# Kernel tuning notes

Hardware: AMD Instinct MI355X
Metric: run time of the kernel (lower is better)

Reference implementation:

```python
import jax, jax.numpy as jnp
import numpy as np

B, K, N, D, H, NNEG, NTOP = 8, 8, 128, 256, 128, 64, 64
UNARY_SCALES = (1.0, 1.0, 1.0)  # one scale per tree level, tree_height = log2(K) = 3


def setup_inputs():
    key = jax.random.key(0)
    ks = jax.random.split(key, 8)
    s = 0.05
    return {
        'pos_fea': jax.random.normal(ks[0], (B, K, N, D), jnp.float32),
        'neg_fea': jax.random.normal(ks[1], (B * K, NNEG, D), jnp.float32),
        'pos_classes': jax.random.randint(ks[2], (B, K, N), 0, 20),
        'target_class': jax.random.randint(ks[3], (B,), 0, 20),
        'Wp1': jax.random.normal(ks[4], (2 * D, H), jnp.float32) * s,
        'bp1': jnp.zeros((H,), jnp.float32),
        'Wp2': jax.random.normal(ks[5], (H, 1), jnp.float32) * s,
        'bp2': jnp.zeros((1,), jnp.float32),
        'Wu1': jax.random.normal(ks[6], (2 * D, H), jnp.float32) * s,
        'bu1': jnp.zeros((H,), jnp.float32),
        'Wu2': jax.random.normal(ks[7], (H, 1), jnp.float32) * s,
        'bu2': jnp.zeros((1,), jnp.float32),
    }


def _relation(f0, f1, W1, b1, W2, b2):
    # RelationModule: Dense(H, relu) -> Dense(1) applied to concat([f0_m, f1_n])
    # for every cross pair; concat-Dense is split into two GEMMs. -> [Bn, M0, M1]
    d = f0.shape[-1]
    h0 = jnp.einsum('bmd,dh->bmh', f0, W1[:d])
    h1 = jnp.einsum('bnd,dh->bnh', f1, W1[d:])
    h = jax.nn.relu(h0[:, :, None, :] + h1[:, None, :, :] + b1)
    return jnp.einsum('bmnh,h->bmn', h, W2[:, 0]) + b2[0]


def _bg(t, idx):
    # batched_gather along axis 1: t [Bn, P, ...], idx [Bn, T]
    ie = idx.reshape(idx.shape + (1,) * (t.ndim - 2))
    ie = jnp.broadcast_to(ie, idx.shape + t.shape[2:])
    return jnp.take_along_axis(t, ie, axis=1)


def _rep(fea, sub):
    # subproblem representative feature: fea [Bn,S,N,D], sub [Bn,M,S] -> [Bn,M,D]
    idx = jnp.swapaxes(sub, 1, 2)[..., None]              # [Bn,S,M,1]
    idx = jnp.broadcast_to(idx, idx.shape[:-1] + (fea.shape[-1],))
    return jnp.take_along_axis(fea, idx, axis=2).mean(axis=1)


def _tree(pos_fea, neg_fea, Wp1, bp1, Wp2, bp2, Wu1, bu1, Wu2, bu2):
    pos_flat = pos_fea.reshape(B * K, N, D)
    # UnaryModule: mean relation score of each positive proposal vs the negative bag
    ue = _relation(pos_flat, neg_fea, Wu1, bu1, Wu2, bu2).mean(-1)   # [B*K, N]
    sub = jnp.broadcast_to(jnp.arange(N, dtype=jnp.int32)[None, :, None], (B * K, N, 1))
    pe = jnp.zeros_like(ue)
    tree_height = int(np.log2(K))
    best = None
    for i in range(tree_height):
        S = 2 ** i                      # subproblem size per branch at this level
        Bn = sub.shape[0] // 2
        M = sub.shape[1]
        sub2 = sub.reshape(Bn, 2, M, S)  # [::2] / [1::2] split of adjacent rows
        sub0, sub1 = sub2[:, 0], sub2[:, 1]
        pe2 = pe.reshape(Bn, 2, M)
        ue2 = ue.reshape(Bn, 2, M)
        fea = pos_flat.reshape(Bn, 2, S, N, D)
        rep0 = _rep(fea[:, 0], sub0)
        rep1 = _rep(fea[:, 1], sub1)
        # PairwiseCrossSimilarity: scores for all cross pairs of candidates
        scores = _relation(rep0, rep1, Wp1, bp1, Wp2, bp2).reshape(Bn, M * M)
        p0 = jnp.repeat(jnp.arange(M), M)
        p1 = jnp.tile(jnp.arange(M), M)
        pe = pe2[:, 0][:, p0] + pe2[:, 1][:, p1] - scores
        ue = ue2[:, 0][:, p0] + ue2[:, 1][:, p1]
        total = pe + UNARY_SCALES[i] * ue
        sub = jnp.concatenate([sub0[:, p0], sub1[:, p1]], axis=-1)  # [Bn, M*M, 2S]
        topk = 1 if i == tree_height - 1 else min(M * M, NTOP)
        _, inds = jax.lax.top_k(-total, topk)
        sub = _bg(sub, inds)
        ue = jnp.take_along_axis(ue, inds, axis=1)
        pe = jnp.take_along_axis(pe, inds, axis=1)
        best = jnp.take_along_axis(total, inds, axis=1)
    return sub, best


def reference(pos_fea, neg_fea, pos_classes, target_class,
              Wp1, bp1, Wp2, bp2, Wu1, bu1, Wu2, bu2):
    sub, _ = _tree(pos_fea, neg_fea, Wp1, bp1, Wp2, bp2, Wu1, bu1, Wu2, bu2)
    is_target = (pos_classes == target_class[:, None, None]).astype(jnp.float32)
    return sub[:, 0], is_target  # selected proposal per image [B,K], [B,K,N]
```

## Files before the change

kernel.cpp:

```cpp
#include <hip/hip_runtime.h>
#include <stdint.h>

#define B_ 8
#define K_ 8
#define N_ 128
#define D_ 256
#define H_ 128
#define NNEG_ 64

typedef unsigned long long u64;
typedef float f4 __attribute__((ext_vector_type(4)));

typedef const __attribute__((address_space(1))) void gvoid;
typedef __attribute__((address_space(3))) void lvoid;
#define G2L(gsrc, ldst) \
    __builtin_amdgcn_global_load_lds((gvoid*)(gsrc), (lvoid*)(ldst), 16, 0, 0)

__device__ __forceinline__ u64 shfl_xor_u64(u64 v, int m) {
    int lo = __shfl_xor((int)(unsigned)v, m, 64);
    int hi = __shfl_xor((int)(unsigned)(v >> 32), m, 64);
    return ((u64)(unsigned)hi << 32) | (unsigned)lo;
}
__device__ __forceinline__ u64 bitonic_merge64(u64 m, int lane) {
#pragma unroll
    for (int j = 32; j > 0; j >>= 1) {
        u64 o = shfl_xor_u64(m, j);
        bool keepMin = ((lane & j) == 0);
        bool lt = m < o;
        m = (keepMin == lt) ? m : o;
    }
    return m;
}
__device__ __forceinline__ u64 merge2(u64 a, u64 b, int lane) {
    u64 br = shfl_xor_u64(b, 63);
    u64 m = a < br ? a : br;
    return bitonic_merge64(m, lane);
}
__device__ __forceinline__ unsigned sortable(float f) {
    unsigned u = __float_as_uint(f);
    return (u & 0x80000000u) ? ~u : (u | 0x80000000u);
}
__device__ __forceinline__ float unsortable(unsigned u) {
    return __uint_as_float((u & 0x80000000u) ? (u & 0x7FFFFFFFu) : ~u);
}
__device__ __forceinline__ void sort128_reg(u64& v0, u64& v1, int lane) {
#pragma unroll
    for (int k = 2; k <= 64; k <<= 1) {
        bool d0 = ((lane & k) == 0);
        bool d1 = (k == 64) ? false : d0;
#pragma unroll
        for (int j = k >> 1; j > 0; j >>= 1) {
            u64 o0 = shfl_xor_u64(v0, j);
            bool km0 = (((lane & j) == 0) == d0);
            v0 = (km0 == (v0 < o0)) ? v0 : o0;
            u64 o1 = shfl_xor_u64(v1, j);
            bool km1 = (((lane & j) == 0) == d1);
            v1 = (km1 == (v1 < o1)) ? v1 : o1;
        }
    }
    if (v0 > v1) { u64 tmp = v0; v0 = v1; v1 = tmp; }
#pragma unroll
    for (int j = 32; j > 0; j >>= 1) {
        bool km = ((lane & j) == 0);
        u64 o0 = shfl_xor_u64(v0, j);
        v0 = (km == (v0 < o0)) ? v0 : o0;
        u64 o1 = shfl_xor_u64(v1, j);
        v1 = (km == (v1 < o1)) ? v1 : o1;
    }
}

__global__ __launch_bounds__(64) void g1_gemm(
    const float* __restrict__ pos, const float* __restrict__ neg,
    const float* __restrict__ Wu1, const float* __restrict__ Wp1,
    const int* __restrict__ pos_classes, const int* __restrict__ target_class,
    float* __restrict__ HU0, float* __restrict__ HU1n,
    float* __restrict__ HP0, float* __restrict__ HP1,
    float* __restrict__ outp) {
    int bid = blockIdx.x;
    int t = threadIdx.x;
    if (bid >= 896) {
        int base = (bid - 896) * 2048 + t * 32;
#pragma unroll
        for (int q = 0; q < 32; ++q) {
            int idx = base + q;
            outp[64 + idx] = (pos_classes[idx] == target_class[idx >> 10]) ? 1.0f : 0.0f;
        }
        return;
    }
    const float* A; const float* W; float* OUT; int bid2;
    if (bid < 256)      { A = pos; W = Wu1;           OUT = HU0;  bid2 = bid; }
    else if (bid < 384) { A = neg; W = Wu1 + D_ * H_; OUT = HU1n; bid2 = bid - 256; }
    else if (bid < 640) { A = pos; W = Wp1;           OUT = HP0;  bid2 = bid - 384; }
    else                { A = pos; W = Wp1 + D_ * H_; OUT = HP1;  bid2 = bid - 640; }
    int rb = (bid2 >> 1) * 64;
    int cb64 = (bid2 & 1) * 64;

    __shared__ __align__(16) float AsL[2][64 * 32];
    __shared__ __align__(16) float BsL[2][32 * 64];
    int tx = t & 7, ty = t >> 3;
    f4 acc[8][2];
#pragma unroll
    for (int i = 0; i < 8; ++i) { acc[i][0] = (f4)0.f; acc[i][1] = (f4)0.f; }

#pragma unroll
    for (int rep = 0; rep < 8; ++rep) {
        int flat = rep * 64 + t;
        int row = flat >> 3;
        int kq = (flat & 7) ^ ((flat >> 5) & 7);
        G2L(&A[(size_t)(rb + row) * D_ + kq * 4], &AsL[0][rep * 256]);
    }
#pragma unroll
    for (int rep = 0; rep < 8; ++rep) {
        int flat = rep * 64 + t;
        int kr = flat >> 4, cq = flat & 15;
        G2L(&W[(size_t)kr * H_ + cb64 + cq * 4], &BsL[0][rep * 256]);
    }
    __syncthreads();

    for (int chunk = 0; chunk < 8; ++chunk) {
        int cur = chunk & 1, nxt = cur ^ 1;
        if (chunk < 7) {
            int k0n = (chunk + 1) * 32;
#pragma unroll
            for (int rep = 0; rep < 8; ++rep) {
                int flat = rep * 64 + t;
                int row = flat >> 3;
                int kq = (flat & 7) ^ ((flat >> 5) & 7);
                G2L(&A[(size_t)(rb + row) * D_ + k0n + kq * 4], &AsL[nxt][rep * 256]);
            }
#pragma unroll
            for (int rep = 0; rep < 8; ++rep) {
                int flat = rep * 64 + t;
                int kr = flat >> 4, cq = flat & 15;
                G2L(&W[(size_t)(k0n + kr) * H_ + cb64 + cq * 4], &BsL[nxt][rep * 256]);
            }
        }
#pragma unroll
        for (int g = 0; g < 8; ++g) {
            f4 av[8];
#pragma unroll
            for (int i = 0; i < 8; ++i) {
                int row = ty * 8 + i;
                int qp = g ^ ((2 * ty + (i >> 2)) & 7);
                av[i] = *(const f4*)&AsL[cur][row * 32 + qp * 4];
            }
#pragma unroll
            for (int q = 0; q < 4; ++q) {
                f4 b0 = *(const f4*)&BsL[cur][(g * 4 + q) * 64 + tx * 8];
                f4 b1 = *(const f4*)&BsL[cur][(g * 4 + q) * 64 + tx * 8 + 4];
#pragma unroll
                for (int i = 0; i < 8; ++i) {
                    float a = av[i][q];
                    acc[i][0][0] += a * b0[0]; acc[i][0][1] += a * b0[1];
                    acc[i][0][2] += a * b0[2]; acc[i][0][3] += a * b0[3];
                    acc[i][1][0] += a * b1[0]; acc[i][1][1] += a * b1[1];
                    acc[i][1][2] += a * b1[2]; acc[i][1][3] += a * b1[3];
                }
            }
        }
        __syncthreads();
    }
#pragma unroll
    for (int i = 0; i < 8; ++i) {
        *(f4*)&OUT[(size_t)(rb + ty * 8 + i) * H_ + cb64 + tx * 8] = acc[i][0];
        *(f4*)&OUT[(size_t)(rb + ty * 8 + i) * H_ + cb64 + tx * 8 + 4] = acc[i][1];
    }
}

__global__ __launch_bounds__(128) void g2_ue_sc0(
    const float* __restrict__ HU0, const float* __restrict__ HU1n,
    const float* __restrict__ bu1, const float* __restrict__ Wu2,
    const float* __restrict__ bu2v,
    const float* __restrict__ HP0, const float* __restrict__ HP1,
    const float* __restrict__ bp1, const float* __restrict__ Wp2,
    const float* __restrict__ bp2,
    float* __restrict__ t0, float* __restrict__ sc0) {
    __shared__ float LsT[128][36];
    __shared__ float RsT[128][68];
    __shared__ float wsv[128];
    __shared__ float red[32][33];

    int bid = blockIdx.x;
    int t = threadIdx.x;
    bool is_ue = bid < 256;

    const float* Lsrc; const float* Rsrc; const float* b1v; const float* W2;
    if (is_ue) {
        int bk = bid >> 2, mt = bid & 3;
        Lsrc = HU0 + (size_t)(bk * N_ + mt * 32) * H_;
        Rsrc = HU1n + (size_t)bk * NNEG_ * H_;
        b1v = bu1; W2 = Wu2;
    } else {
        int bid2 = bid - 256;
        int b = bid2 >> 3, m0t = (bid2 >> 1) & 3, m1t = bid2 & 1;
        Lsrc = HP0 + (size_t)b * 2 * N_ * H_ + m0t * 32 * H_;
        Rsrc = HP1 + (size_t)b * 2 * N_ * H_ + N_ * H_ + m1t * 64 * H_;
        b1v = bp1; W2 = Wp2;
    }
    for (int i = t; i < 32 * 32; i += 128) {
        int m = i & 31, hq = i >> 5;
        const f4 a = *(const f4*)&Lsrc[(size_t)m * H_ + hq * 4];
        const f4 b = *(const f4*)&b1v[hq * 4];
        LsT[hq * 4 + 0][m] = a[0] + b[0];
        LsT[hq * 4 + 1][m] = a[1] + b[1];
        LsT[hq * 4 + 2][m] = a[2] + b[2];
        LsT[hq * 4 + 3][m] = a[3] + b[3];
    }
    for (int i = t; i < 64 * 32; i += 128) {
        int n = i & 63, hq = i >> 6;
        const f4 a = *(const f4*)&Rsrc[(size_t)n * H_ + hq * 4];
        RsT[hq * 4 + 0][n] = a[0];
        RsT[hq * 4 + 1][n] = a[1];
        RsT[hq * 4 + 2][n] = a[2];
        RsT[hq * 4 + 3][n] = a[3];
    }
    wsv[t] = W2[t];
    __syncthreads();

    int tm = t & 7, tn = t >> 3;
    f4 acc[4];
#pragma unroll
    for (int i = 0; i < 4; ++i) acc[i] = (f4)0.f;
#pragma unroll 2
    for (int hg = 0; hg < 32; ++hg) {
        f4 wv = *(const f4*)&wsv[hg * 4];
        f4 lv[4], rv[4];
#pragma unroll
        for (int s = 0; s < 4; ++s) {
            lv[s] = *(const f4*)&LsT[hg * 4 + s][tm * 4];
            rv[s] = *(const f4*)&RsT[hg * 4 + s][tn * 4];
        }
#pragma unroll
        for (int s = 0; s < 4; ++s) {
            float w = wv[s];
#pragma unroll
            for (int i = 0; i < 4; ++i) {
                float l = lv[s][i];
                float v;
                v = l + rv[s][0]; v = v > 0.f ? v : 0.f; acc[i][0] += v * w;
                v = l + rv[s][1]; v = v > 0.f ? v : 0.f; acc[i][1] += v * w;
                v = l + rv[s][2]; v = v > 0.f ? v : 0.f; acc[i][2] += v * w;
                v = l + rv[s][3]; v = v > 0.f ? v : 0.f; acc[i][3] += v * w;
            }
        }
    }

    if (is_ue) {
        int bk = bid >> 2, mt = bid & 3;
#pragma unroll
        for (int i = 0; i < 4; ++i) {
            red[tm * 4 + i][tn * 2 + 0] = acc[i][0] + acc[i][1];
            red[tm * 4 + i][tn * 2 + 1] = acc[i][2] + acc[i][3];
        }
        __syncthreads();
        if (t < 32) {
            float s = 0.f;
            for (int q = 0; q < 32; ++q) s += red[t][q];
            t0[bk * N_ + mt * 32 + t] = s * (1.0f / NNEG_) + bu2v[0];
        }
    } else {
        int bid2 = bid - 256;
        int b = bid2 >> 3, m0t = (bid2 >> 1) & 3, m1t = bid2 & 1;
        float bp2v = bp2[0];
        float* orow = sc0 + (size_t)b * 16384;
#pragma unroll
        for (int i = 0; i < 4; ++i) {
            int m0 = m0t * 32 + tm * 4 + i;
            int m1 = m1t * 64 + tn * 4;
            f4 o = {acc[i][0] + bp2v, acc[i][1] + bp2v,
                    acc[i][2] + bp2v, acc[i][3] + bp2v};
            *(f4*)&orow[m0 * 128 + m1] = o;
        }
    }
}

__global__ __launch_bounds__(256) void g3a_top0(const float* __restrict__ sc0,
                                                const float* __restrict__ t0,
                                                u64* __restrict__ g3c) {
    int bid = blockIdx.x;
    int r = bid >> 3, c = bid & 7;
    int t = threadIdx.x, lane = t & 63, w = t >> 6;
    __shared__ float tt[256];
    __shared__ u64 cand[4][128];
    if (t < 256) tt[t] = t0[r * 256 + t];
    __syncthreads();
    const float* row = sc0 + (size_t)r * 16384 + c * 2048 + w * 512;
    unsigned sv[8];
#pragma unroll
    for (int j = 0; j < 8; ++j) {
        int li = j * 64 + lane;
        int idx = c * 2048 + w * 512 + li;
        float v = (tt[idx >> 7] + tt[128 + (idx & 127)]) - row[li];
        sv[j] = sortable(v);
    }
    unsigned T = 0u;
#pragma unroll
    for (int it = 0; it < 16; ++it) {
        int p = 30 - 2 * it;
        unsigned C1 = T | (1u << p), C2 = T | (2u << p), C3 = T | (3u << p);
        unsigned c1 = 0u, c2 = 0u, c3 = 0u;
#pragma unroll
        for (int j = 0; j < 8; ++j) {
            c1 += (unsigned)__popcll(__ballot(sv[j] < C1));
            c2 += (unsigned)__popcll(__ballot(sv[j] < C2));
            c3 += (unsigned)__popcll(__ballot(sv[j] < C3));
        }
        unsigned k = (c3 < 64u) ? 3u : (c2 < 64u) ? 2u : (c1 < 64u) ? 1u : 0u;
        T |= (k << p);
    }
    u64* my = cand[w];
    int base = 0;
#pragma unroll
    for (int j = 0; j < 8; ++j) {
        u64 mask = __ballot(sv[j] <= T);
        if (sv[j] <= T) {
            int pos = base + (int)__popcll(mask & ((1ull << lane) - 1ull));
            if (pos < 128) {
                int idx = c * 2048 + w * 512 + j * 64 + lane;
                my[pos] = ((u64)sv[j] << 32) | (unsigned)idx;
            }
        }
        base += (int)__popcll(mask);
    }
    int cc = base < 128 ? base : 128;
    u64 v0 = (lane < cc) ? my[lane] : ~0ull;
    u64 v1 = (64 + lane < cc) ? my[64 + lane] : ~0ull;
    sort128_reg(v0, v1, lane);
    my[lane] = v0;
    __syncthreads();
    if (w == 0) {
        u64 x0 = cand[0][lane], x1 = cand[1][lane];
        u64 x2 = cand[2][lane], x3 = cand[3][lane];
        u64 y0 = merge2(x0, x1, lane), y1 = merge2(x2, x3, lane);
        g3c[(size_t)bid * 64 + lane] = merge2(y0, y1, lane);
    }
}

__global__ __launch_bounds__(256) void g4a_s1(
    const float* __restrict__ HP0, const float* __restrict__ HP1,
    const u64* __restrict__ g3c, int* __restrict__ pA,
    const float* __restrict__ bp1, const float* __restrict__ Wp2,
    const float* __restrict__ bp2, u64* __restrict__ g4top) {
    int bid = blockIdx.x;
    int u = bid >> 3, mq = (bid >> 1) & 3, nh = bid & 1;
    int t = threadIdx.x, lane = t & 63, w = t >> 6;
    __shared__ float LsT[128][17];
    __shared__ float RsT[128][34];
    __shared__ float taL[64], taR[64];
    __shared__ int paL[64], paR[64];
    __shared__ float wsv[128];
    __shared__ u64 cand[4][64];
    if (w < 2) {
        const u64* Lp = g3c + (size_t)(2 * u + w) * 512;
        u64 x0 = Lp[lane], x1 = Lp[64 + lane], x2 = Lp[128 + lane], x3 = Lp[192 + lane];
        u64 x4 = Lp[256 + lane], x5 = Lp[320 + lane], x6 = Lp[384 + lane], x7 = Lp[448 + lane];
        u64 y0 = merge2(x0, x1, lane), y1 = merge2(x2, x3, lane);
        u64 y2 = merge2(x4, x5, lane), y3 = merge2(x6, x7, lane);
        u64 z0 = merge2(y0, y1, lane), z1 = merge2(y2, y3, lane);
        u64 f = merge2(z0, z1, lane);
        int idx = (int)(f & 0xFFFFFFFFull);
        int pk = ((idx >> 7) << 8) | (idx & 127);
        float tv = unsortable((unsigned)(f >> 32));
        if (w == 0) { taL[lane] = tv; paL[lane] = pk; }
        else        { taR[lane] = tv; paR[lane] = pk; }
    }
    if (t >= 128) wsv[t - 128] = Wp2[t - 128];
    float bp2v = bp2[0];
    __syncthreads();
    if ((bid & 7) == 0) {
        if (t < 64) pA[(2 * u) * 64 + t] = paL[t];
        else if (t < 128) pA[(2 * u + 1) * 64 + (t - 64)] = paR[t - 64];
    }
    for (int i = t; i < 16 * 128; i += 256) {
        int m = i >> 7, h = i & 127;
        int pk = paL[mq * 16 + m]; int a0 = pk >> 8, a1 = pk & 255;
        float s = HP0[(size_t)(4 * u) * 16384 + a0 * 128 + h]
                + HP0[(size_t)(4 * u + 1) * 16384 + a1 * 128 + h];
        LsT[h][m] = s * 0.5f + bp1[h];
    }
    for (int i = t; i < 32 * 128; i += 256) {
        int n = i >> 7, h = i & 127;
        int pk = paR[nh * 32 + n]; int c0 = pk >> 8, c1 = pk & 255;
        float s = HP1[(size_t)(4 * u + 2) * 16384 + c0 * 128 + h]
                + HP1[(size_t)(4 * u + 3) * 16384 + c1 * 128 + h];
        RsT[h][n] = s * 0.5f;
    }
    __syncthreads();
    int lm = w * 4 + (lane >> 4);
    int ln = lane & 15;
    float a0 = 0.f, a1 = 0.f;
#pragma unroll 4
    for (int h = 0; h < 128; ++h) {
        float lv = LsT[h][lm];
        const float2 rv = *(const float2*)&RsT[h][ln * 2];
        float wv = wsv[h];
        float v;
        v = lv + rv.x; v = v > 0.f ? v : 0.f; a0 += v * wv;
        v = lv + rv.y; v = v > 0.f ? v : 0.f; a1 += v * wv;
    }
    int m_unit = mq * 16 + lm;
    int n0 = nh * 32 + ln * 2;
    float val0 = (taL[mq * 16 + lm] + taR[nh * 32 + ln * 2 + 0]) - (a0 + bp2v);
    float val1 = (taL[mq * 16 + lm] + taR[nh * 32 + ln * 2 + 1]) - (a1 + bp2v);
    u64 v0 = ((u64)sortable(val0) << 32) | (unsigned)(m_unit * 64 + n0);
    u64 v1 = ((u64)sortable(val1) << 32) | (unsigned)(m_unit * 64 + n0 + 1);
    sort128_reg(v0, v1, lane);
    cand[w][lane] = v0;
    __syncthreads();
    if (w == 0) {
        u64 x0 = cand[0][lane], x1 = cand[1][lane];
        u64 x2 = cand[2][lane], x3 = cand[3][lane];
        u64 y0 = merge2(x0, x1, lane), y1 = merge2(x2, x3, lane);
        g4top[(size_t)bid * 64 + lane] = merge2(y0, y1, lane);
    }
}

__global__ __launch_bounds__(512) void g4b_s2(
    const float* __restrict__ HP0, const float* __restrict__ HP1,
    const int* __restrict__ pA, const u64* __restrict__ g4top,
    const float* __restrict__ bp1, const float* __restrict__ Wp2,
    const float* __restrict__ bp2, float* __restrict__ outp) {
    int b = blockIdx.x;
    int t = threadIdx.x, lane = t & 63, w = t >> 6;
    __shared__ float LsT[128][68];
    __shared__ float RsT[128][68];
    __shared__ float tL[64], tR[64];
    __shared__ unsigned subL[64], subR[64];
    __shared__ float wsv[128];
    __shared__ u64 sred[8];
    if (t < 128) wsv[t] = Wp2[t];
    float bp2v = bp2[0];
    if (w < 2) {
        const u64* Lp = g4top + (size_t)(2 * b + w) * 512;
        u64 x0 = Lp[lane], x1 = Lp[64 + lane], x2 = Lp[128 + lane], x3 = Lp[192 + lane];
        u64 x4 = Lp[256 + lane], x5 = Lp[320 + lane], x6 = Lp[384 + lane], x7 = Lp[448 + lane];
        u64 y0 = merge2(x0, x1, lane), y1 = merge2(x2, x3, lane);
        u64 y2 = merge2(x4, x5, lane), y3 = merge2(x6, x7, lane);
        u64 z0 = merge2(y0, y1, lane), z1 = merge2(y2, y3, lane);
        u64 m = merge2(z0, z1, lane);
        int idx = (int)(m & 0xFFFFFFFFull);
        int p0 = idx >> 6, p1 = idx & 63;
        float val = unsortable((unsigned)(m >> 32));
        int rowL = 4 * b + 2 * w;
        int pkL = pA[rowL * 64 + p0];
        int pkR = pA[(rowL + 1) * 64 + p1];
        unsigned leaves = ((unsigned)pkL << 16) | (unsigned)pkR;
        if (w == 0) { tL[lane] = val; subL[lane] = leaves; }
        else        { tR[lane] = val; subR[lane] = leaves; }
    }
    __syncthreads();
    for (int i = t; i < 64 * 128; i += 512) {
        int m = i >> 7, h = i & 127;
        unsigned s4 = subL[m];
        float s = HP0[(size_t)(8 * b + 0) * 16384 + ((s4 >> 24) & 255u) * 128 + h]
                + HP0[(size_t)(8 * b + 1) * 16384 + ((s4 >> 16) & 255u) * 128 + h]
                + HP0[(size_t)(8 * b + 2) * 16384 + ((s4 >> 8) & 255u) * 128 + h]
                + HP0[(size_t)(8 * b + 3) * 16384 + (s4 & 255u) * 128 + h];
        LsT[h][m] = s * 0.25f + bp1[h];
    }
    for (int i = t; i < 64 * 128; i += 512) {
        int n = i >> 7, h = i & 127;
        unsigned s4 = subR[n];
        float s = HP1[(size_t)(8 * b + 4) * 16384 + ((s4 >> 24) & 255u) * 128 + h]
                + HP1[(size_t)(8 * b + 5) * 16384 + ((s4 >> 16) & 255u) * 128 + h]
                + HP1[(size_t)(8 * b + 6) * 16384 + ((s4 >> 8) & 255u) * 128 + h]
                + HP1[(size_t)(8 * b + 7) * 16384 + (s4 & 255u) * 128 + h];
        RsT[h][n] = s * 0.25f;
    }
    __syncthreads();
    int qm = (w & 3) * 4 + (lane >> 4);
    int qn = (w >> 2) * 16 + (lane & 15);
    float acc[4][2];
#pragma unroll
    for (int i = 0; i < 4; ++i) { acc[i][0] = 0.f; acc[i][1] = 0.f; }
#pragma unroll 2
    for (int h = 0; h < 128; ++h) {
        const float4 lv = *(const float4*)&LsT[h][qm * 4];
        const float2 rv = *(const float2*)&RsT[h][qn * 2];
        float wv = wsv[h];
        float v;
        v = lv.x + rv.x; v = v > 0.f ? v : 0.f; acc[0][0] += v * wv;
        v = lv.x + rv.y; v = v > 0.f ? v : 0.f; acc[0][1] += v * wv;
        v = lv.y + rv.x; v = v > 0.f ? v : 0.f; acc[1][0] += v * wv;
        v = lv.y + rv.y; v = v > 0.f ? v : 0.f; acc[1][1] += v * wv;
        v = lv.z + rv.x; v = v > 0.f ? v : 0.f; acc[2][0] += v * wv;
        v = lv.z + rv.y; v = v > 0.f ? v : 0.f; acc[2][1] += v * wv;
        v = lv.w + rv.x; v = v > 0.f ? v : 0.f; acc[3][0] += v * wv;
        v = lv.w + rv.y; v = v > 0.f ? v : 0.f; acc[3][1] += v * wv;
    }
    u64 best = ~0ull;
#pragma unroll
    for (int mi = 0; mi < 4; ++mi) {
#pragma unroll
        for (int nj = 0; nj < 2; ++nj) {
            int m = qm * 4 + mi;
            int ng = qn * 2 + nj;
            float val = (tL[m] + tR[ng]) - (acc[mi][nj] + bp2v);
            u64 kk = ((u64)sortable(val) << 32) | (unsigned)(m * 64 + ng);
            best = kk < best ? kk : best;
        }
    }
#pragma unroll
    for (int off = 32; off > 0; off >>= 1) {
        u64 o = shfl_xor_u64(best, off);
        best = o < best ? o : best;
    }
    if (lane == 0) sred[w] = best;
    __syncthreads();
    if (t == 0) {
        u64 bb = sred[0];
        for (int p = 1; p < 8; ++p) { u64 o = sred[p]; bb = o < bb ? o : bb; }
        int idx = (int)(bb & 0xFFFFFFFFull);
        unsigned sl = subL[idx >> 6], sr = subR[idx & 63];
        outp[b * 8 + 0] = (float)((sl >> 24) & 255u);
        outp[b * 8 + 1] = (float)((sl >> 16) & 255u);
        outp[b * 8 + 2] = (float)((sl >> 8) & 255u);
        outp[b * 8 + 3] = (float)(sl & 255u);
        outp[b * 8 + 4] = (float)((sr >> 24) & 255u);
        outp[b * 8 + 5] = (float)((sr >> 16) & 255u);
        outp[b * 8 + 6] = (float)((sr >> 8) & 255u);
        outp[b * 8 + 7] = (float)(sr & 255u);
    }
}

extern "C" void kernel_launch(void* const* d_in, const int* in_sizes, int n_in,
                              void* d_out, int out_size, void* d_ws, size_t ws_size,
                              hipStream_t stream) {
    const float* pos = (const float*)d_in[0];
    const float* neg = (const float*)d_in[1];
    const int* pos_classes = (const int*)d_in[2];
    const int* target_class = (const int*)d_in[3];
    const float* Wp1 = (const float*)d_in[4];
    const float* bp1 = (const float*)d_in[5];
    const float* Wp2 = (const float*)d_in[6];
    const float* bp2 = (const float*)d_in[7];
    const float* Wu1 = (const float*)d_in[8];
    const float* bu1 = (const float*)d_in[9];
    const float* Wu2 = (const float*)d_in[10];
    const float* bu2 = (const float*)d_in[11];

    float* wsf = (float*)d_ws;
    float* HU0 = wsf;
    float* HP0 = HU0 + 1048576;
    float* HP1 = HP0 + 1048576;
    float* HU1n = HP1 + 1048576;
    float* t0 = HU1n + 524288;
    float* sc0 = t0 + 8192;
    int* pA = (int*)(sc0 + 524288);
    u64* g3c = (u64*)wsf;
    u64* g4top = (u64*)wsf + 16384;
    float* outp = (float*)d_out;

    g1_gemm<<<900, 64, 0, stream>>>(pos, neg, Wu1, Wp1, pos_classes,
                                    target_class, HU0, HU1n, HP0, HP1, outp);
    g2_ue_sc0<<<512, 128, 0, stream>>>(HU0, HU1n, bu1, Wu2, bu2,
                                       HP0, HP1, bp1, Wp2, bp2, t0, sc0);
    g3a_top0<<<256, 256, 0, stream>>>(sc0, t0, g3c);
    g4a_s1<<<128, 256, 0, stream>>>(HP0, HP1, g3c, pA, bp1, Wp2, bp2, g4top);
    g4b_s2<<<8, 512, 0, stream>>>(HP0, HP1, pA, g4top, bp1, Wp2, bp2, outp);
}
```

Baseline: 172.1 us.

## Split-K the projection GEMM into two partial buffers summed by consumers

```diff
diff --git a/kernel.cpp b/kernel.cpp
--- a/kernel.cpp
+++ b/kernel.cpp
@@ -15,6 +15,9 @@
 typedef __attribute__((address_space(3))) void lvoid;
 #define G2L(gsrc, ldst) \
     __builtin_amdgcn_global_load_lds((gvoid*)(gsrc), (lvoid*)(ldst), 16, 0, 0)
+
+#define PSZ_BIG 1048576
+#define PSZ_NEG 524288
 
 __device__ __forceinline__ u64 shfl_xor_u64(u64 v, int m) {
     int lo = __shfl_xor((int)(unsigned)v, m, 64);
@@ -73,13 +76,13 @@
     const float* __restrict__ pos, const float* __restrict__ neg,
     const float* __restrict__ Wu1, const float* __restrict__ Wp1,
     const int* __restrict__ pos_classes, const int* __restrict__ target_class,
-    float* __restrict__ HU0, float* __restrict__ HU1n,
-    float* __restrict__ HP0, float* __restrict__ HP1,
+    float* __restrict__ HU0p, float* __restrict__ HU1np,
+    float* __restrict__ HP0p, float* __restrict__ HP1p,
     float* __restrict__ outp) {
     int bid = blockIdx.x;
     int t = threadIdx.x;
-    if (bid >= 896) {
-        int base = (bid - 896) * 2048 + t * 32;
+    if (bid >= 1792) {
+        int base = (bid - 1792) * 2048 + t * 32;
 #pragma unroll
         for (int q = 0; q < 32; ++q) {
             int idx = base + q;
@@ -87,67 +90,69 @@
         }
         return;
     }
-    const float* A; const float* W; float* OUT; int bid2;
-    if (bid < 256)      { A = pos; W = Wu1;           OUT = HU0;  bid2 = bid; }
-    else if (bid < 384) { A = neg; W = Wu1 + D_ * H_; OUT = HU1n; bid2 = bid - 256; }
-    else if (bid < 640) { A = pos; W = Wp1;           OUT = HP0;  bid2 = bid - 384; }
-    else                { A = pos; W = Wp1 + D_ * H_; OUT = HP1;  bid2 = bid - 640; }
-    int rb = (bid2 >> 1) * 64;
-    int cb64 = (bid2 & 1) * 64;
-
-    __shared__ __align__(16) float AsL[2][64 * 32];
-    __shared__ __align__(16) float BsL[2][32 * 64];
+    const float* A; const float* W; float* OUT; int bid2; int psz;
+    if (bid < 512)       { A = pos; W = Wu1;           OUT = HU0p;  bid2 = bid;        psz = PSZ_BIG; }
+    else if (bid < 768)  { A = neg; W = Wu1 + D_ * H_; OUT = HU1np; bid2 = bid - 512;  psz = PSZ_NEG; }
+    else if (bid < 1280) { A = pos; W = Wp1;           OUT = HP0p;  bid2 = bid - 768;  psz = PSZ_BIG; }
+    else                 { A = pos; W = Wp1 + D_ * H_; OUT = HP1p;  bid2 = bid - 1280; psz = PSZ_BIG; }
+    int tile = bid2 >> 1, khalf = bid2 & 1;
+    int rb = (tile >> 1) * 64;
+    int cb64 = (tile & 1) * 64;
+    int kbase = khalf * 128;
+    OUT += (size_t)khalf * psz;
+
+    __shared__ __align__(16) float AsL[2][64 * 16];
+    __shared__ __align__(16) float BsL[2][16 * 64];
     int tx = t & 7, ty = t >> 3;
     f4 acc[8][2];
 #pragma unroll
     for (int i = 0; i < 8; ++i) { acc[i][0] = (f4)0.f; acc[i][1] = (f4)0.f; }
 
 #pragma unroll
-    for (int rep = 0; rep < 8; ++rep) {
+    for (int rep = 0; rep < 4; ++rep) {
         int flat = rep * 64 + t;
-        int row = flat >> 3;
-        int kq = (flat & 7) ^ ((flat >> 5) & 7);
-        G2L(&A[(size_t)(rb + row) * D_ + kq * 4], &AsL[0][rep * 256]);
-    }
-#pragma unroll
-    for (int rep = 0; rep < 8; ++rep) {
+        int row = flat >> 2;
+        int kq = (flat & 3) ^ ((flat >> 5) & 3);
+        G2L(&A[(size_t)(rb + row) * D_ + kbase + kq * 4], &AsL[0][rep * 256]);
+    }
+#pragma unroll
+    for (int rep = 0; rep < 4; ++rep) {
         int flat = rep * 64 + t;
         int kr = flat >> 4, cq = flat & 15;
-        G2L(&W[(size_t)kr * H_ + cb64 + cq * 4], &BsL[0][rep * 256]);
+        G2L(&W[(size_t)(kbase + kr) * H_ + cb64 + cq * 4], &BsL[0][rep * 256]);
     }
     __syncthreads();
 
     for (int chunk = 0; chunk < 8; ++chunk) {
         int cur = chunk & 1, nxt = cur ^ 1;
         if (chunk < 7) {
-            int k0n = (chunk + 1) * 32;
-#pragma unroll
-            for (int rep = 0; rep < 8; ++rep) {
+            int k0n = kbase + (chunk + 1) * 16;
+#pragma unroll
+            for (int rep = 0; rep < 4; ++rep) {
                 int flat = rep * 64 + t;
-                int row = flat >> 3;
-                int kq = (flat & 7) ^ ((flat >> 5) & 7);
+                int row = flat >> 2;
+                int kq = (flat & 3) ^ ((flat >> 5) & 3);
                 G2L(&A[(size_t)(rb + row) * D_ + k0n + kq * 4], &AsL[nxt][rep * 256]);
             }
 #pragma unroll
-            for (int rep = 0; rep < 8; ++rep) {
+            for (int rep = 0; rep < 4; ++rep) {
                 int flat = rep * 64 + t;
                 int kr = flat >> 4, cq = flat & 15;
                 G2L(&W[(size_t)(k0n + kr) * H_ + cb64 + cq * 4], &BsL[nxt][rep * 256]);
             }
         }
 #pragma unroll
-        for (int g = 0; g < 8; ++g) {
+        for (int g = 0; g < 4; ++g) {
+            int qp = g ^ (ty & 3);
             f4 av[8];
 #pragma unroll
-            for (int i = 0; i < 8; ++i) {
-                int row = ty * 8 + i;
-                int qp = g ^ ((2 * ty + (i >> 2)) & 7);
-                av[i] = *(const f4*)&AsL[cur][row * 32 + qp * 4];
-            }
+            for (int i = 0; i < 8; ++i)
+                av[i] = *(const f4*)&AsL[cur][(ty * 8 + i) * 16 + qp * 4];
 #pragma unroll
             for (int q = 0; q < 4; ++q) {
-                f4 b0 = *(const f4*)&BsL[cur][(g * 4 + q) * 64 + tx * 8];
-                f4 b1 = *(const f4*)&BsL[cur][(g * 4 + q) * 64 + tx * 8 + 4];
+                int kk = g * 4 + q;
+                f4 b0 = *(const f4*)&BsL[cur][kk * 64 + tx * 8];
+                f4 b1 = *(const f4*)&BsL[cur][kk * 64 + tx * 8 + 4];
 #pragma unroll
                 for (int i = 0; i < 8; ++i) {
                     float a = av[i][q];
@@ -168,10 +173,10 @@
 }
 
 __global__ __launch_bounds__(128) void g2_ue_sc0(
-    const float* __restrict__ HU0, const float* __restrict__ HU1n,
+    const float* __restrict__ HU0p, const float* __restrict__ HU1np,
     const float* __restrict__ bu1, const float* __restrict__ Wu2,
     const float* __restrict__ bu2v,
-    const float* __restrict__ HP0, const float* __restrict__ HP1,
+    const float* __restrict__ HP0p, const float* __restrict__ HP1p,
     const float* __restrict__ bp1, const float* __restrict__ Wp2,
     const float* __restrict__ bp2,
     float* __restrict__ t0, float* __restrict__ sc0) {
@@ -185,34 +190,37 @@
     bool is_ue = bid < 256;
 
     const float* Lsrc; const float* Rsrc; const float* b1v; const float* W2;
+    int Lofs, Rofs;
     if (is_ue) {
         int bk = bid >> 2, mt = bid & 3;
-        Lsrc = HU0 + (size_t)(bk * N_ + mt * 32) * H_;
-        Rsrc = HU1n + (size_t)bk * NNEG_ * H_;
+        Lsrc = HU0p + (size_t)(bk * N_ + mt * 32) * H_;  Lofs = PSZ_BIG;
+        Rsrc = HU1np + (size_t)bk * NNEG_ * H_;          Rofs = PSZ_NEG;
         b1v = bu1; W2 = Wu2;
     } else {
         int bid2 = bid - 256;
         int b = bid2 >> 3, m0t = (bid2 >> 1) & 3, m1t = bid2 & 1;
-        Lsrc = HP0 + (size_t)b * 2 * N_ * H_ + m0t * 32 * H_;
-        Rsrc = HP1 + (size_t)b * 2 * N_ * H_ + N_ * H_ + m1t * 64 * H_;
+        Lsrc = HP0p + (size_t)b * 2 * N_ * H_ + m0t * 32 * H_;           Lofs = PSZ_BIG;
+        Rsrc = HP1p + (size_t)b * 2 * N_ * H_ + N_ * H_ + m1t * 64 * H_; Rofs = PSZ_BIG;
         b1v = bp1; W2 = Wp2;
     }
     for (int i = t; i < 32 * 32; i += 128) {
         int m = i & 31, hq = i >> 5;
         const f4 a = *(const f4*)&Lsrc[(size_t)m * H_ + hq * 4];
+        const f4 a2 = *(const f4*)&Lsrc[(size_t)m * H_ + hq * 4 + Lofs];
         const f4 b = *(const f4*)&b1v[hq * 4];
-        LsT[hq * 4 + 0][m] = a[0] + b[0];
-        LsT[hq * 4 + 1][m] = a[1] + b[1];
-        LsT[hq * 4 + 2][m] = a[2] + b[2];
-        LsT[hq * 4 + 3][m] = a[3] + b[3];
+        LsT[hq * 4 + 0][m] = (a[0] + a2[0]) + b[0];
+        LsT[hq * 4 + 1][m] = (a[1] + a2[1]) + b[1];
+        LsT[hq * 4 + 2][m] = (a[2] + a2[2]) + b[2];
+        LsT[hq * 4 + 3][m] = (a[3] + a2[3]) + b[3];
     }
     for (int i = t; i < 64 * 32; i += 128) {
         int n = i & 63, hq = i >> 6;
         const f4 a = *(const f4*)&Rsrc[(size_t)n * H_ + hq * 4];
-        RsT[hq * 4 + 0][n] = a[0];
-        RsT[hq * 4 + 1][n] = a[1];
-        RsT[hq * 4 + 2][n] = a[2];
-        RsT[hq * 4 + 3][n] = a[3];
+        const f4 a2 = *(const f4*)&Rsrc[(size_t)n * H_ + hq * 4 + Rofs];
+        RsT[hq * 4 + 0][n] = a[0] + a2[0];
+        RsT[hq * 4 + 1][n] = a[1] + a2[1];
+        RsT[hq * 4 + 2][n] = a[2] + a2[2];
+        RsT[hq * 4 + 3][n] = a[3] + a2[3];
     }
     wsv[t] = W2[t];
     __syncthreads();
@@ -337,7 +345,7 @@
 }
 
 __global__ __launch_bounds__(256) void g4a_s1(
-    const float* __restrict__ HP0, const float* __restrict__ HP1,
+    const float* __restrict__ HP0p, const float* __restrict__ HP1p,
     const u64* __restrict__ g3c, int* __restrict__ pA,
     const float* __restrict__ bp1, const float* __restrict__ Wp2,
     const float* __restrict__ bp2, u64* __restrict__ g4top) {
@@ -374,15 +382,19 @@
     for (int i = t; i < 16 * 128; i += 256) {
         int m = i >> 7, h = i & 127;
         int pk = paL[mq * 16 + m]; int a0 = pk >> 8, a1 = pk & 255;
-        float s = HP0[(size_t)(4 * u) * 16384 + a0 * 128 + h]
-                + HP0[(size_t)(4 * u + 1) * 16384 + a1 * 128 + h];
+        size_t i0 = (size_t)(4 * u) * 16384 + a0 * 128 + h;
+        size_t i1 = (size_t)(4 * u + 1) * 16384 + a1 * 128 + h;
+        float s = (HP0p[i0] + HP0p[i0 + PSZ_BIG])
+                + (HP0p[i1] + HP0p[i1 + PSZ_BIG]);
         LsT[h][m] = s * 0.5f + bp1[h];
     }
     for (int i = t; i < 32 * 128; i += 256) {
         int n = i >> 7, h = i & 127;
         int pk = paR[nh * 32 + n]; int c0 = pk >> 8, c1 = pk & 255;
-        float s = HP1[(size_t)(4 * u + 2) * 16384 + c0 * 128 + h]
-                + HP1[(size_t)(4 * u + 3) * 16384 + c1 * 128 + h];
+        size_t i0 = (size_t)(4 * u + 2) * 16384 + c0 * 128 + h;
+        size_t i1 = (size_t)(4 * u + 3) * 16384 + c1 * 128 + h;
+        float s = (HP1p[i0] + HP1p[i0 + PSZ_BIG])
+                + (HP1p[i1] + HP1p[i1 + PSZ_BIG]);
         RsT[h][n] = s * 0.5f;
     }
     __syncthreads();
@@ -416,7 +428,7 @@
 }
 
 __global__ __launch_bounds__(512) void g4b_s2(
-    const float* __restrict__ HP0, const float* __restrict__ HP1,
+    const float* __restrict__ HP0p, const float* __restrict__ HP1p,
     const int* __restrict__ pA, const u64* __restrict__ g4top,
     const float* __restrict__ bp1, const float* __restrict__ Wp2,
     const float* __restrict__ bp2, float* __restrict__ outp) {
@@ -452,19 +464,27 @@
     for (int i = t; i < 64 * 128; i += 512) {
         int m = i >> 7, h = i & 127;
         unsigned s4 = subL[m];
-        float s = HP0[(size_t)(8 * b + 0) * 16384 + ((s4 >> 24) & 255u) * 128 + h]
-                + HP0[(size_t)(8 * b + 1) * 16384 + ((s4 >> 16) & 255u) * 128 + h]
-                + HP0[(size_t)(8 * b + 2) * 16384 + ((s4 >> 8) & 255u) * 128 + h]
-                + HP0[(size_t)(8 * b + 3) * 16384 + (s4 & 255u) * 128 + h];
+        size_t j0 = (size_t)(8 * b + 0) * 16384 + ((s4 >> 24) & 255u) * 128 + h;
+        size_t j1 = (size_t)(8 * b + 1) * 16384 + ((s4 >> 16) & 255u) * 128 + h;
+        size_t j2 = (size_t)(8 * b + 2) * 16384 + ((s4 >> 8) & 255u) * 128 + h;
+        size_t j3 = (size_t)(8 * b + 3) * 16384 + (s4 & 255u) * 128 + h;
+        float s = (HP0p[j0] + HP0p[j0 + PSZ_BIG])
+                + (HP0p[j1] + HP0p[j1 + PSZ_BIG])
+                + (HP0p[j2] + HP0p[j2 + PSZ_BIG])
+                + (HP0p[j3] + HP0p[j3 + PSZ_BIG]);
         LsT[h][m] = s * 0.25f + bp1[h];
     }
     for (int i = t; i < 64 * 128; i += 512) {
         int n = i >> 7, h = i & 127;
         unsigned s4 = subR[n];
-        float s = HP1[(size_t)(8 * b + 4) * 16384 + ((s4 >> 24) & 255u) * 128 + h]
-                + HP1[(size_t)(8 * b + 5) * 16384 + ((s4 >> 16) & 255u) * 128 + h]
-                + HP1[(size_t)(8 * b + 6) * 16384 + ((s4 >> 8) & 255u) * 128 + h]
-                + HP1[(size_t)(8 * b + 7) * 16384 + (s4 & 255u) * 128 + h];
+        size_t j0 = (size_t)(8 * b + 4) * 16384 + ((s4 >> 24) & 255u) * 128 + h;
+        size_t j1 = (size_t)(8 * b + 5) * 16384 + ((s4 >> 16) & 255u) * 128 + h;
+        size_t j2 = (size_t)(8 * b + 6) * 16384 + ((s4 >> 8) & 255u) * 128 + h;
+        size_t j3 = (size_t)(8 * b + 7) * 16384 + (s4 & 255u) * 128 + h;
+        float s = (HP1p[j0] + HP1p[j0 + PSZ_BIG])
+                + (HP1p[j1] + HP1p[j1 + PSZ_BIG])
+                + (HP1p[j2] + HP1p[j2 + PSZ_BIG])
+                + (HP1p[j3] + HP1p[j3 + PSZ_BIG]);
         RsT[h][n] = s * 0.25f;
     }
     __syncthreads();
@@ -540,22 +560,22 @@
     const float* bu2 = (const float*)d_in[11];
 
     float* wsf = (float*)d_ws;
-    float* HU0 = wsf;
-    float* HP0 = HU0 + 1048576;
-    float* HP1 = HP0 + 1048576;
-    float* HU1n = HP1 + 1048576;
-    float* t0 = HU1n + 524288;
+    float* HU0p = wsf;
+    float* HP0p = HU0p + 2 * PSZ_BIG;
+    float* HP1p = HP0p + 2 * PSZ_BIG;
+    float* HU1np = HP1p + 2 * PSZ_BIG;
+    float* t0 = HU1np + 2 * PSZ_NEG;
     float* sc0 = t0 + 8192;
     int* pA = (int*)(sc0 + 524288);
     u64* g3c = (u64*)wsf;
     u64* g4top = (u64*)wsf + 16384;
     float* outp = (float*)d_out;
 
-    g1_gemm<<<900, 64, 0, stream>>>(pos, neg, Wu1, Wp1, pos_classes,
-                                    target_class, HU0, HU1n, HP0, HP1, outp);
-    g2_ue_sc0<<<512, 128, 0, stream>>>(HU0, HU1n, bu1, Wu2, bu2,
-                                       HP0, HP1, bp1, Wp2, bp2, t0, sc0);
+    g1_gemm<<<1796, 64, 0, stream>>>(pos, neg, Wu1, Wp1, pos_classes,
+                                     target_class, HU0p, HU1np, HP0p, HP1p, outp);
+    g2_ue_sc0<<<512, 128, 0, stream>>>(HU0p, HU1np, bu1, Wu2, bu2,
+                                       HP0p, HP1p, bp1, Wp2, bp2, t0, sc0);
     g3a_top0<<<256, 256, 0, stream>>>(sc0, t0, g3c);
-    g4a_s1<<<128, 256, 0, stream>>>(HP0, HP1, g3c, pA, bp1, Wp2, bp2, g4top);
-    g4b_s2<<<8, 512, 0, stream>>>(HP0, HP1, pA, g4top, bp1, Wp2, bp2, outp);
-}
+    g4a_s1<<<128, 256, 0, stream>>>(HP0p, HP1p, g3c, pA, bp1, Wp2, bp2, g4top);
+    g4b_s2<<<8, 512, 0, stream>>>(HP0p, HP1p, pA, g4top, bp1, Wp2, bp2, outp);
+}
```

Result: no change. 170.5 us (-0.9%).
